# Optimization experiments

Measured on AMD Instinct MI355X. Metric: run time of the kernel, lower is better.

Reference implementation:

```python
import jax, jax.numpy as jnp
import numpy as np

# Sizes: B graphs, NPG nodes per graph (equal segments -> to_dense_batch == reshape),
# M instructions, DN node feat dim, DQ question dim.
B, NPG, M, DN, DQ = 64, 4096, 8, 512, 256
N = B * NPG
RATIO = 0.3
K = int(np.ceil(RATIO * NPG))  # pyg topk with ratio<1 keeps ceil(ratio*n) nodes per graph


def setup_inputs() -> dict:
    key = jax.random.key(0)
    ks = jax.random.split(key, 4)
    x = jax.random.normal(ks[0], (N, DN), jnp.float32)
    u = jax.random.normal(ks[1], (M, B, DQ), jnp.float32)
    Wn = jax.random.normal(ks[2], (DN, DQ), jnp.float32) / np.sqrt(DN)
    bn = jnp.zeros((DQ,), jnp.float32)
    batch = jnp.repeat(jnp.arange(B, dtype=jnp.int32), NPG)  # sorted graph ids, equal segments
    edge_index = jax.random.randint(ks[3], (2, 4 * N), 0, N, dtype=jnp.int32)  # unused by forward
    return {"x": x, "u": u, "Wn": Wn, "bn": bn, "batch": batch, "edge_index": edge_index}


def reference(x, u, Wn, bn, batch, edge_index):
    # node_nn: Linear(DN, DQ) + exact GELU (torch.nn.GELU default)
    h = jax.nn.gelu(x @ Wn + bn, approximate=False)            # [N, DQ]
    # to_dense_batch with equal-size graphs == reshape, mask all True
    hb = h.reshape(B, NPG, DQ)                                  # [B, n, D]
    inst = jnp.transpose(u, (1, 0, 2))                          # [B, M, D]
    scores = jnp.einsum('bmd,bnd->bmn', inst, hb)               # [B, M, n]
    attn = jax.nn.softmax(scores, axis=2)
    gate = attn.sum(axis=1)                                     # [B, n]  (gate[batch_mask] flatten)
    # per-graph ratio top-k -> hard binary mask (index_fill_ 1 at top-k, 0 elsewhere)
    kth = jax.lax.top_k(gate, K)[0][:, -1:]                     # k-th largest per graph
    mask = (gate >= kth).astype(h.dtype)                        # [B, n]
    return mask.reshape(N)
```

## Files before the change

### kernel.cpp

```cpp
#include <hip/hip_runtime.h>
#include <math.h>

#define B_     64
#define NPG_   4096
#define M_     8
#define DN_    512
#define DQ_    256
#define N_     (B_*NPG_)
#define KSEL_  1229

typedef _Float16 f16x4  __attribute__((ext_vector_type(4)));
typedef _Float16 f16x8  __attribute__((ext_vector_type(8)));
typedef float    f32x16 __attribute__((ext_vector_type(16)));

__global__ __launch_bounds__(256) void k_prep(const float* __restrict__ Wn,
                                              _Float16* __restrict__ th,
                                              _Float16* __restrict__ tl)
{
    const int k = blockIdx.x;
    const int c = threadIdx.x;
    const float w = Wn[k * DQ_ + c];
    const _Float16 h = (_Float16)w;
    th[c * DN_ + k] = h;
    tl[c * DN_ + k] = (_Float16)(w - (float)h);
}

__global__ __launch_bounds__(256, 2) void k_score(
    const float* __restrict__ x, const float* __restrict__ u,
    const float* __restrict__ bn,
    const _Float16* __restrict__ wth, const _Float16* __restrict__ wtl,
    float* __restrict__ scores)
{
    __shared__ __align__(16) _Float16 Ahi[128][40], Alo[128][40];
    __shared__ __align__(16) _Float16 Bhi[256][40], Blo[256][40];
    __shared__ float usS[M_][DQ_];
    __shared__ float bnsS[DQ_];
    __shared__ float part2[2][128][M_];

    const int tid = threadIdx.x;
    const int ln  = tid & 63;
    const int w   = tid >> 6;
    const int wr  = w >> 1;
    const int wc  = w & 1;
    const int lr  = ln & 31;
    const int lh  = ln >> 5;
    const int row0 = blockIdx.x * 128;
    const int b    = row0 >> 12;

    #pragma unroll
    for (int p = 0; p < 8; ++p) {
        const int idx = p * 256 + tid;
        usS[idx >> 8][idx & 255] = u[((idx >> 8) * B_ + b) * DQ_ + (idx & 255)];
    }
    bnsS[tid] = bn[tid];

    const int arow = tid >> 1;
    const int aks  = (tid & 1) * 16;
    const float*  xp  = x + (long)(row0 + arow) * DN_ + aks;
    const float4* bhp = (const float4*)(wth + (long)tid * DN_);
    const float4* blp = (const float4*)(wtl + (long)tid * DN_);

    float4 xa[4], bh[4], bl[4];
    #pragma unroll
    for (int i = 0; i < 4; ++i) {
        xa[i] = ((const float4*)xp)[i];
        bh[i] = bhp[i];
        bl[i] = blp[i];
    }

    f32x16 acc[2][4];
    #pragma unroll
    for (int mt = 0; mt < 2; ++mt)
        #pragma unroll
        for (int nt = 0; nt < 4; ++nt)
            #pragma unroll
            for (int r = 0; r < 16; ++r) acc[mt][nt][r] = 0.0f;

    for (int kt = 0; kt < DN_ / 32; ++kt) {
        __syncthreads();

        #pragma unroll
        for (int i = 0; i < 4; ++i) {
            const float4 v = xa[i];
            f16x4 h, lo2;
            h[0] = (_Float16)v.x; lo2[0] = (_Float16)(v.x - (float)h[0]);
            h[1] = (_Float16)v.y; lo2[1] = (_Float16)(v.y - (float)h[1]);
            h[2] = (_Float16)v.z; lo2[2] = (_Float16)(v.z - (float)h[2]);
            h[3] = (_Float16)v.w; lo2[3] = (_Float16)(v.w - (float)h[3]);
            *(f16x4*)&Ahi[arow][aks + 4 * i] = h;
            *(f16x4*)&Alo[arow][aks + 4 * i] = lo2;
        }
        #pragma unroll
        for (int i = 0; i < 4; ++i) {
            *(float4*)&Bhi[tid][i * 8] = bh[i];
            *(float4*)&Blo[tid][i * 8] = bl[i];
        }
        __syncthreads();

        if (kt + 1 < DN_ / 32) {
            const float* xn = xp + (kt + 1) * 32;
            #pragma unroll
            for (int i = 0; i < 4; ++i) {
                xa[i] = ((const float4*)xn)[i];
                bh[i] = bhp[(kt + 1) * 4 + i];
                bl[i] = blp[(kt + 1) * 4 + i];
            }
        }

        #pragma unroll
        for (int s = 0; s < 2; ++s) {
            const int o = s * 16 + lh * 8;
            f16x8 afh[2], afl[2], bfh[4], bfl[4];
            #pragma unroll
            for (int mt = 0; mt < 2; ++mt) {
                const int r = wr * 64 + mt * 32 + lr;
                afh[mt] = *(const f16x8*)&Ahi[r][o];
                afl[mt] = *(const f16x8*)&Alo[r][o];
            }
            #pragma unroll
            for (int nt = 0; nt < 4; ++nt) {
                const int c = wc * 128 + nt * 32 + lr;
                bfh[nt] = *(const f16x8*)&Bhi[c][o];
                bfl[nt] = *(const f16x8*)&Blo[c][o];
            }
            #pragma unroll
            for (int mt = 0; mt < 2; ++mt)
                #pragma unroll
                for (int nt = 0; nt < 4; ++nt) {
                    acc[mt][nt] = __builtin_amdgcn_mfma_f32_32x32x16_f16(
                        afh[mt], bfh[nt], acc[mt][nt], 0, 0, 0);
                    acc[mt][nt] = __builtin_amdgcn_mfma_f32_32x32x16_f16(
                        afh[mt], bfl[nt], acc[mt][nt], 0, 0, 0);
                    acc[mt][nt] = __builtin_amdgcn_mfma_f32_32x32x16_f16(
                        afl[mt], bfh[nt], acc[mt][nt], 0, 0, 0);
                }
        }
    }

    #pragma unroll
    for (int mt = 0; mt < 2; ++mt)
        #pragma unroll
        for (int nt = 0; nt < 4; ++nt) {
            const float bnc = bnsS[wc * 128 + nt * 32 + lr];
            #pragma unroll
            for (int r = 0; r < 16; ++r) {
                const float z = acc[mt][nt][r] + bnc;
                acc[mt][nt][r] = 0.5f * z * (1.0f + erff(z * 0.7071067811865476f));
            }
        }

    #pragma unroll 1
    for (int m = 0; m < 8; ++m) {
        const float u0 = usS[m][wc * 128 +   0 + lr];
        const float u1 = usS[m][wc * 128 +  32 + lr];
        const float u2 = usS[m][wc * 128 +  64 + lr];
        const float u3 = usS[m][wc * 128 +  96 + lr];
        float p[2][16];
        #pragma unroll
        for (int mt = 0; mt < 2; ++mt)
            #pragma unroll
            for (int r = 0; r < 16; ++r)
                p[mt][r] = acc[mt][0][r] * u0 + acc[mt][1][r] * u1
                         + acc[mt][2][r] * u2 + acc[mt][3][r] * u3;
        #pragma unroll
        for (int mask = 1; mask < 32; mask <<= 1)
            #pragma unroll
            for (int mt = 0; mt < 2; ++mt)
                #pragma unroll
                for (int r = 0; r < 16; ++r)
                    p[mt][r] += __shfl_xor(p[mt][r], mask, 64);
        if (lr == m) {
            #pragma unroll
            for (int mt = 0; mt < 2; ++mt)
                #pragma unroll
                for (int r = 0; r < 16; ++r) {
                    const int row = wr * 64 + mt * 32 + (r & 3) + 8 * (r >> 2) + 4 * lh;
                    part2[wc][row][m] = p[mt][r];
                }
        }
    }
    __syncthreads();

    #pragma unroll
    for (int i = 0; i < 4; ++i) {
        const int idx = i * 256 + tid;
        const int row = idx >> 3, m = idx & 7;
        scores[(long)(row0 + row) * M_ + m] = part2[0][row][m] + part2[1][row][m];
    }
}

__global__ __launch_bounds__(256) void k_mask(
    const float* __restrict__ scores, float* __restrict__ out)
{
    __shared__ float red[256];
    __shared__ float gateLDS[NPG_];
    __shared__ float gmaxS[M_];
    __shared__ float ginvS[M_];
    __shared__ unsigned hist[256];
    __shared__ unsigned sPrefix;
    __shared__ int sWant;

    const int b   = blockIdx.x;
    const int tid = threadIdx.x;
    const float* sb = scores + (long)b * NPG_ * M_;

    float lmax[8];
    #pragma unroll
    for (int m = 0; m < 8; ++m) lmax[m] = -INFINITY;
    for (int it = 0; it < 16; ++it) {
        const int n = it * 256 + tid;
        const float4 s0 = *(const float4*)(sb + (long)n * 8);
        const float4 s1 = *(const float4*)(sb + (long)n * 8 + 4);
        lmax[0] = fmaxf(lmax[0], s0.x); lmax[1] = fmaxf(lmax[1], s0.y);
        lmax[2] = fmaxf(lmax[2], s0.z); lmax[3] = fmaxf(lmax[3], s0.w);
        lmax[4] = fmaxf(lmax[4], s1.x); lmax[5] = fmaxf(lmax[5], s1.y);
        lmax[6] = fmaxf(lmax[6], s1.z); lmax[7] = fmaxf(lmax[7], s1.w);
    }
    for (int m = 0; m < 8; ++m) {
        red[tid] = lmax[m]; __syncthreads();
        for (int s = 128; s > 0; s >>= 1) {
            if (tid < s) red[tid] = fmaxf(red[tid], red[tid + s]);
            __syncthreads();
        }
        if (tid == 0) gmaxS[m] = red[0];
        __syncthreads();
    }

    float lsum[8];
    #pragma unroll
    for (int m = 0; m < 8; ++m) lsum[m] = 0.0f;
    for (int it = 0; it < 16; ++it) {
        const int n = it * 256 + tid;
        const float4 s0 = *(const float4*)(sb + (long)n * 8);
        const float4 s1 = *(const float4*)(sb + (long)n * 8 + 4);
        lsum[0] += expf(s0.x - gmaxS[0]); lsum[1] += expf(s0.y - gmaxS[1]);
        lsum[2] += expf(s0.z - gmaxS[2]); lsum[3] += expf(s0.w - gmaxS[3]);
        lsum[4] += expf(s1.x - gmaxS[4]); lsum[5] += expf(s1.y - gmaxS[5]);
        lsum[6] += expf(s1.z - gmaxS[6]); lsum[7] += expf(s1.w - gmaxS[7]);
    }
    for (int m = 0; m < 8; ++m) {
        red[tid] = lsum[m]; __syncthreads();
        for (int s = 128; s > 0; s >>= 1) {
            if (tid < s) red[tid] += red[tid + s];
            __syncthreads();
        }
        if (tid == 0) ginvS[m] = 1.0f / red[0];
        __syncthreads();
    }

    for (int it = 0; it < 16; ++it) {
        const int n = it * 256 + tid;
        const float4 s0 = *(const float4*)(sb + (long)n * 8);
        const float4 s1 = *(const float4*)(sb + (long)n * 8 + 4);
        float g = 0.0f;
        g += expf(s0.x - gmaxS[0]) * ginvS[0];
        g += expf(s0.y - gmaxS[1]) * ginvS[1];
        g += expf(s0.z - gmaxS[2]) * ginvS[2];
        g += expf(s0.w - gmaxS[3]) * ginvS[3];
        g += expf(s1.x - gmaxS[4]) * ginvS[4];
        g += expf(s1.y - gmaxS[5]) * ginvS[5];
        g += expf(s1.z - gmaxS[6]) * ginvS[6];
        g += expf(s1.w - gmaxS[7]) * ginvS[7];
        gateLDS[n] = g;
    }
    __syncthreads();

    if (tid == 0) { sPrefix = 0u; sWant = KSEL_; }
    __syncthreads();
    const unsigned himask[4] = {0u, 0xFF000000u, 0xFFFF0000u, 0xFFFFFF00u};
    for (int r = 0; r < 4; ++r) {
        hist[tid] = 0u;
        __syncthreads();
        const unsigned pfx = sPrefix;
        const unsigned hm  = himask[r];
        const int shift = 24 - 8 * r;
        for (int it = 0; it < 16; ++it) {
            const unsigned uv = __float_as_uint(gateLDS[it * 256 + tid]);
            if ((uv & hm) == pfx)
                atomicAdd(&hist[(uv >> shift) & 255u], 1u);
        }
        __syncthreads();
        if (tid == 0) {
            int want = sWant;
            unsigned acc = 0u;
            for (int bb = 255; bb >= 0; --bb) {
                const unsigned h = hist[bb];
                if (acc + h >= (unsigned)want) {
                    sWant   = want - (int)acc;
                    sPrefix = pfx | ((unsigned)bb << shift);
                    break;
                }
                acc += h;
            }
        }
        __syncthreads();
    }
    const float kth = __uint_as_float(sPrefix);

    for (int it = 0; it < 16; ++it) {
        const int n = it * 256 + tid;
        out[(long)b * NPG_ + n] = (gateLDS[n] >= kth) ? 1.0f : 0.0f;
    }
}

extern "C" void kernel_launch(void* const* d_in, const int* in_sizes, int n_in,
                              void* d_out, int out_size, void* d_ws, size_t ws_size,
                              hipStream_t stream) {
    const float* x  = (const float*)d_in[0];
    const float* u  = (const float*)d_in[1];
    const float* Wn = (const float*)d_in[2];
    const float* bn = (const float*)d_in[3];

    float* scores = (float*)d_ws;

    _Float16* wth = (_Float16*)d_out;
    _Float16* wtl = wth + DQ_ * DN_;
    float* out    = (float*)d_out;

    k_prep <<<DN_, 256, 0, stream>>>(Wn, wth, wtl);
    k_score<<<N_ / 128, 256, 0, stream>>>(x, u, bn, wth, wtl, scores);
    k_mask <<<B_, 256, 0, stream>>>(scores, out);
}
```

Before: 1.392 ms.

## Halve score-kernel row tile and widen mask kernel with wave-shuffle reductions

The score kernel now processes 64 rows per block, with each of four waves owning a 64-column slice of the output, which reduces accumulator registers and doubles the grid. Cross-wave partial scores are combined through reused B-tile shared memory. The mask kernel moves to 1024 threads and replaces the tree reductions in shared memory with wave shuffles plus a small cross-wave pass. The trade-off is higher B-tile reload traffic and more LDS reads and shuffles per MFMA in exchange for better occupancy.

Measured after the change: 1.394 ms. No clear change (+0.1%).

```diff
diff --git a/kernel.cpp b/kernel.cpp
--- a/kernel.cpp
+++ b/kernel.cpp
@@ -31,20 +31,18 @@
     const _Float16* __restrict__ wth, const _Float16* __restrict__ wtl,
     float* __restrict__ scores)
 {
-    __shared__ __align__(16) _Float16 Ahi[128][40], Alo[128][40];
+    __shared__ __align__(16) _Float16 Ahi[64][40],  Alo[64][40];
     __shared__ __align__(16) _Float16 Bhi[256][40], Blo[256][40];
     __shared__ float usS[M_][DQ_];
     __shared__ float bnsS[DQ_];
-    __shared__ float part2[2][128][M_];
+    float* part4f = (float*)&Bhi[0][0];
 
     const int tid = threadIdx.x;
     const int ln  = tid & 63;
-    const int w   = tid >> 6;
-    const int wr  = w >> 1;
-    const int wc  = w & 1;
+    const int wc  = tid >> 6;
     const int lr  = ln & 31;
     const int lh  = ln >> 5;
-    const int row0 = blockIdx.x * 128;
+    const int row0 = blockIdx.x * 64;
     const int b    = row0 >> 12;
 
     #pragma unroll
@@ -54,79 +52,79 @@
     }
     bnsS[tid] = bn[tid];
 
-    const int arow = tid >> 1;
-    const int aks  = (tid & 1) * 16;
-    const float*  xp  = x + (long)(row0 + arow) * DN_ + aks;
+    const int arow  = tid >> 2;
+    const int akoff = (tid & 3) * 8;
+    const float*  xp  = x + (long)(row0 + arow) * DN_ + akoff;
     const float4* bhp = (const float4*)(wth + (long)tid * DN_);
     const float4* blp = (const float4*)(wtl + (long)tid * DN_);
 
-    float4 xa[4], bh[4], bl[4];
-    #pragma unroll
-    for (int i = 0; i < 4; ++i) {
-        xa[i] = ((const float4*)xp)[i];
-        bh[i] = bhp[i];
-        bl[i] = blp[i];
-    }
-
-    f32x16 acc[2][4];
+    float4 xa[2], bh[4], bl[4];
+    #pragma unroll
+    for (int i = 0; i < 2; ++i) xa[i] = ((const float4*)xp)[i];
+    #pragma unroll
+    for (int j = 0; j < 4; ++j) { bh[j] = bhp[j]; bl[j] = blp[j]; }
+
+    f32x16 acc[2][2];
     #pragma unroll
     for (int mt = 0; mt < 2; ++mt)
         #pragma unroll
-        for (int nt = 0; nt < 4; ++nt)
+        for (int nt = 0; nt < 2; ++nt)
             #pragma unroll
             for (int r = 0; r < 16; ++r) acc[mt][nt][r] = 0.0f;
 
     for (int kt = 0; kt < DN_ / 32; ++kt) {
         __syncthreads();
 
-        #pragma unroll
-        for (int i = 0; i < 4; ++i) {
-            const float4 v = xa[i];
-            f16x4 h, lo2;
-            h[0] = (_Float16)v.x; lo2[0] = (_Float16)(v.x - (float)h[0]);
-            h[1] = (_Float16)v.y; lo2[1] = (_Float16)(v.y - (float)h[1]);
-            h[2] = (_Float16)v.z; lo2[2] = (_Float16)(v.z - (float)h[2]);
-            h[3] = (_Float16)v.w; lo2[3] = (_Float16)(v.w - (float)h[3]);
-            *(f16x4*)&Ahi[arow][aks + 4 * i] = h;
-            *(f16x4*)&Alo[arow][aks + 4 * i] = lo2;
-        }
-        #pragma unroll
-        for (int i = 0; i < 4; ++i) {
-            *(float4*)&Bhi[tid][i * 8] = bh[i];
-            *(float4*)&Blo[tid][i * 8] = bl[i];
+        {
+            f16x8 h, l;
+            h[0] = (_Float16)xa[0].x; l[0] = (_Float16)(xa[0].x - (float)h[0]);
+            h[1] = (_Float16)xa[0].y; l[1] = (_Float16)(xa[0].y - (float)h[1]);
+            h[2] = (_Float16)xa[0].z; l[2] = (_Float16)(xa[0].z - (float)h[2]);
+            h[3] = (_Float16)xa[0].w; l[3] = (_Float16)(xa[0].w - (float)h[3]);
+            h[4] = (_Float16)xa[1].x; l[4] = (_Float16)(xa[1].x - (float)h[4]);
+            h[5] = (_Float16)xa[1].y; l[5] = (_Float16)(xa[1].y - (float)h[5]);
+            h[6] = (_Float16)xa[1].z; l[6] = (_Float16)(xa[1].z - (float)h[6]);
+            h[7] = (_Float16)xa[1].w; l[7] = (_Float16)(xa[1].w - (float)h[7]);
+            *(f16x8*)&Ahi[arow][akoff] = h;
+            *(f16x8*)&Alo[arow][akoff] = l;
+        }
+        #pragma unroll
+        for (int j = 0; j < 4; ++j) {
+            *(float4*)&Bhi[tid][j * 8] = bh[j];
+            *(float4*)&Blo[tid][j * 8] = bl[j];
         }
         __syncthreads();
 
         if (kt + 1 < DN_ / 32) {
             const float* xn = xp + (kt + 1) * 32;
             #pragma unroll
-            for (int i = 0; i < 4; ++i) {
-                xa[i] = ((const float4*)xn)[i];
-                bh[i] = bhp[(kt + 1) * 4 + i];
-                bl[i] = blp[(kt + 1) * 4 + i];
+            for (int i = 0; i < 2; ++i) xa[i] = ((const float4*)xn)[i];
+            #pragma unroll
+            for (int j = 0; j < 4; ++j) {
+                bh[j] = bhp[(kt + 1) * 4 + j];
+                bl[j] = blp[(kt + 1) * 4 + j];
             }
         }
 
         #pragma unroll
         for (int s = 0; s < 2; ++s) {
             const int o = s * 16 + lh * 8;
-            f16x8 afh[2], afl[2], bfh[4], bfl[4];
+            f16x8 afh[2], afl[2], bfh[2], bfl[2];
             #pragma unroll
             for (int mt = 0; mt < 2; ++mt) {
-                const int r = wr * 64 + mt * 32 + lr;
-                afh[mt] = *(const f16x8*)&Ahi[r][o];
-                afl[mt] = *(const f16x8*)&Alo[r][o];
-            }
-            #pragma unroll
-            for (int nt = 0; nt < 4; ++nt) {
-                const int c = wc * 128 + nt * 32 + lr;
+                afh[mt] = *(const f16x8*)&Ahi[mt * 32 + lr][o];
+                afl[mt] = *(const f16x8*)&Alo[mt * 32 + lr][o];
+            }
+            #pragma unroll
+            for (int nt = 0; nt < 2; ++nt) {
+                const int c = wc * 64 + nt * 32 + lr;
                 bfh[nt] = *(const f16x8*)&Bhi[c][o];
                 bfl[nt] = *(const f16x8*)&Blo[c][o];
             }
             #pragma unroll
             for (int mt = 0; mt < 2; ++mt)
                 #pragma unroll
-                for (int nt = 0; nt < 4; ++nt) {
+                for (int nt = 0; nt < 2; ++nt) {
                     acc[mt][nt] = __builtin_amdgcn_mfma_f32_32x32x16_f16(
                         afh[mt], bfh[nt], acc[mt][nt], 0, 0, 0);
                     acc[mt][nt] = __builtin_amdgcn_mfma_f32_32x32x16_f16(
@@ -140,8 +138,8 @@
     #pragma unroll
     for (int mt = 0; mt < 2; ++mt)
         #pragma unroll
-        for (int nt = 0; nt < 4; ++nt) {
-            const float bnc = bnsS[wc * 128 + nt * 32 + lr];
+        for (int nt = 0; nt < 2; ++nt) {
+            const float bnc = bnsS[wc * 64 + nt * 32 + lr];
             #pragma unroll
             for (int r = 0; r < 16; ++r) {
                 const float z = acc[mt][nt][r] + bnc;
@@ -149,19 +147,18 @@
             }
         }
 
+    __syncthreads();
+
     #pragma unroll 1
     for (int m = 0; m < 8; ++m) {
-        const float u0 = usS[m][wc * 128 +   0 + lr];
-        const float u1 = usS[m][wc * 128 +  32 + lr];
-        const float u2 = usS[m][wc * 128 +  64 + lr];
-        const float u3 = usS[m][wc * 128 +  96 + lr];
+        const float u0 = usS[m][wc * 64 +  0 + lr];
+        const float u1 = usS[m][wc * 64 + 32 + lr];
         float p[2][16];
         #pragma unroll
         for (int mt = 0; mt < 2; ++mt)
             #pragma unroll
             for (int r = 0; r < 16; ++r)
-                p[mt][r] = acc[mt][0][r] * u0 + acc[mt][1][r] * u1
-                         + acc[mt][2][r] * u2 + acc[mt][3][r] * u3;
+                p[mt][r] = acc[mt][0][r] * u0 + acc[mt][1][r] * u1;
         #pragma unroll
         for (int mask = 1; mask < 32; mask <<= 1)
             #pragma unroll
@@ -174,108 +171,137 @@
             for (int mt = 0; mt < 2; ++mt)
                 #pragma unroll
                 for (int r = 0; r < 16; ++r) {
-                    const int row = wr * 64 + mt * 32 + (r & 3) + 8 * (r >> 2) + 4 * lh;
-                    part2[wc][row][m] = p[mt][r];
+                    const int row = mt * 32 + (r & 3) + 8 * (r >> 2) + 4 * lh;
+                    part4f[(wc * 64 + row) * M_ + m] = p[mt][r];
                 }
         }
     }
     __syncthreads();
 
     #pragma unroll
-    for (int i = 0; i < 4; ++i) {
+    for (int i = 0; i < 2; ++i) {
         const int idx = i * 256 + tid;
         const int row = idx >> 3, m = idx & 7;
-        scores[(long)(row0 + row) * M_ + m] = part2[0][row][m] + part2[1][row][m];
+        const float v = part4f[(  0 + row) * M_ + m] + part4f[( 64 + row) * M_ + m]
+                      + part4f[(128 + row) * M_ + m] + part4f[(192 + row) * M_ + m];
+        scores[(long)(row0 + row) * M_ + m] = v;
     }
 }
 
-__global__ __launch_bounds__(256) void k_mask(
+__global__ __launch_bounds__(1024) void k_mask(
     const float* __restrict__ scores, float* __restrict__ out)
 {
-    __shared__ float red[256];
     __shared__ float gateLDS[NPG_];
+    __shared__ float wred[16][M_];
     __shared__ float gmaxS[M_];
     __shared__ float ginvS[M_];
     __shared__ unsigned hist[256];
     __shared__ unsigned sPrefix;
     __shared__ int sWant;
 
-    const int b   = blockIdx.x;
-    const int tid = threadIdx.x;
+    const int b    = blockIdx.x;
+    const int tid  = threadIdx.x;
+    const int wid  = tid >> 6;
+    const int lane = tid & 63;
     const float* sb = scores + (long)b * NPG_ * M_;
 
-    float lmax[8];
-    #pragma unroll
-    for (int m = 0; m < 8; ++m) lmax[m] = -INFINITY;
-    for (int it = 0; it < 16; ++it) {
-        const int n = it * 256 + tid;
+    float lv[8];
+    #pragma unroll
+    for (int m = 0; m < 8; ++m) lv[m] = -INFINITY;
+    #pragma unroll
+    for (int it = 0; it < 4; ++it) {
+        const int n = it * 1024 + tid;
         const float4 s0 = *(const float4*)(sb + (long)n * 8);
         const float4 s1 = *(const float4*)(sb + (long)n * 8 + 4);
-        lmax[0] = fmaxf(lmax[0], s0.x); lmax[1] = fmaxf(lmax[1], s0.y);
-        lmax[2] = fmaxf(lmax[2], s0.z); lmax[3] = fmaxf(lmax[3], s0.w);
-        lmax[4] = fmaxf(lmax[4], s1.x); lmax[5] = fmaxf(lmax[5], s1.y);
-        lmax[6] = fmaxf(lmax[6], s1.z); lmax[7] = fmaxf(lmax[7], s1.w);
-    }
-    for (int m = 0; m < 8; ++m) {
-        red[tid] = lmax[m]; __syncthreads();
-        for (int s = 128; s > 0; s >>= 1) {
-            if (tid < s) red[tid] = fmaxf(red[tid], red[tid + s]);
-            __syncthreads();
-        }
-        if (tid == 0) gmaxS[m] = red[0];
-        __syncthreads();
-    }
-
-    float lsum[8];
-    #pragma unroll
-    for (int m = 0; m < 8; ++m) lsum[m] = 0.0f;
-    for (int it = 0; it < 16; ++it) {
-        const int n = it * 256 + tid;
+        lv[0] = fmaxf(lv[0], s0.x); lv[1] = fmaxf(lv[1], s0.y);
+        lv[2] = fmaxf(lv[2], s0.z); lv[3] = fmaxf(lv[3], s0.w);
+        lv[4] = fmaxf(lv[4], s1.x); lv[5] = fmaxf(lv[5], s1.y);
+        lv[6] = fmaxf(lv[6], s1.z); lv[7] = fmaxf(lv[7], s1.w);
+    }
+    #pragma unroll
+    for (int mask = 1; mask < 64; mask <<= 1)
+        #pragma unroll
+        for (int m = 0; m < 8; ++m)
+            lv[m] = fmaxf(lv[m], __shfl_xor(lv[m], mask, 64));
+    if (lane == 0)
+        #pragma unroll
+        for (int m = 0; m < 8; ++m) wred[wid][m] = lv[m];
+    __syncthreads();
+    if (tid < 8) {
+        float mm = -INFINITY;
+        for (int wv = 0; wv < 16; ++wv) mm = fmaxf(mm, wred[wv][tid]);
+        gmaxS[tid] = mm;
+    }
+    __syncthreads();
+
+    float gm[8];
+    #pragma unroll
+    for (int m = 0; m < 8; ++m) gm[m] = gmaxS[m];
+
+    float ls[8];
+    #pragma unroll
+    for (int m = 0; m < 8; ++m) ls[m] = 0.0f;
+    #pragma unroll
+    for (int it = 0; it < 4; ++it) {
+        const int n = it * 1024 + tid;
         const float4 s0 = *(const float4*)(sb + (long)n * 8);
         const float4 s1 = *(const float4*)(sb + (long)n * 8 + 4);
-        lsum[0] += expf(s0.x - gmaxS[0]); lsum[1] += expf(s0.y - gmaxS[1]);
-        lsum[2] += expf(s0.z - gmaxS[2]); lsum[3] += expf(s0.w - gmaxS[3]);
-        lsum[4] += expf(s1.x - gmaxS[4]); lsum[5] += expf(s1.y - gmaxS[5]);
-        lsum[6] += expf(s1.z - gmaxS[6]); lsum[7] += expf(s1.w - gmaxS[7]);
-    }
-    for (int m = 0; m < 8; ++m) {
-        red[tid] = lsum[m]; __syncthreads();
-        for (int s = 128; s > 0; s >>= 1) {
-            if (tid < s) red[tid] += red[tid + s];
-            __syncthreads();
-        }
-        if (tid == 0) ginvS[m] = 1.0f / red[0];
-        __syncthreads();
-    }
-
-    for (int it = 0; it < 16; ++it) {
-        const int n = it * 256 + tid;
+        ls[0] += expf(s0.x - gm[0]); ls[1] += expf(s0.y - gm[1]);
+        ls[2] += expf(s0.z - gm[2]); ls[3] += expf(s0.w - gm[3]);
+        ls[4] += expf(s1.x - gm[4]); ls[5] += expf(s1.y - gm[5]);
+        ls[6] += expf(s1.z - gm[6]); ls[7] += expf(s1.w - gm[7]);
+    }
+    #pragma unroll
+    for (int mask = 1; mask < 64; mask <<= 1)
+        #pragma unroll
+        for (int m = 0; m < 8; ++m)
+            ls[m] += __shfl_xor(ls[m], mask, 64);
+    if (lane == 0)
+        #pragma unroll
+        for (int m = 0; m < 8; ++m) wred[wid][m] = ls[m];
+    __syncthreads();
+    if (tid < 8) {
+        float ss = 0.0f;
+        for (int wv = 0; wv < 16; ++wv) ss += wred[wv][tid];
+        ginvS[tid] = 1.0f / ss;
+    }
+    __syncthreads();
+
+    float gi[8];
+    #pragma unroll
+    for (int m = 0; m < 8; ++m) gi[m] = ginvS[m];
+
+    #pragma unroll
+    for (int it = 0; it < 4; ++it) {
+        const int n = it * 1024 + tid;
         const float4 s0 = *(const float4*)(sb + (long)n * 8);
         const float4 s1 = *(const float4*)(sb + (long)n * 8 + 4);
         float g = 0.0f;
-        g += expf(s0.x - gmaxS[0]) * ginvS[0];
-        g += expf(s0.y - gmaxS[1]) * ginvS[1];
-        g += expf(s0.z - gmaxS[2]) * ginvS[2];
-        g += expf(s0.w - gmaxS[3]) * ginvS[3];
-        g += expf(s1.x - gmaxS[4]) * ginvS[4];
-        g += expf(s1.y - gmaxS[5]) * ginvS[5];
-        g += expf(s1.z - gmaxS[6]) * ginvS[6];
-        g += expf(s1.w - gmaxS[7]) * ginvS[7];
+        g += expf(s0.x - gm[0]) * gi[0];
+        g += expf(s0.y - gm[1]) * gi[1];
+        g += expf(s0.z - gm[2]) * gi[2];
+        g += expf(s0.w - gm[3]) * gi[3];
+        g += expf(s1.x - gm[4]) * gi[4];
+        g += expf(s1.y - gm[5]) * gi[5];
+        g += expf(s1.z - gm[6]) * gi[6];
+        g += expf(s1.w - gm[7]) * gi[7];
         gateLDS[n] = g;
     }
-    __syncthreads();
-
     if (tid == 0) { sPrefix = 0u; sWant = KSEL_; }
     __syncthreads();
-    const unsigned himask[4] = {0u, 0xFF000000u, 0xFFFF0000u, 0xFFFFFF00u};
+
+    #pragma unroll 1
     for (int r = 0; r < 4; ++r) {
-        hist[tid] = 0u;
+        if (tid < 256) hist[tid] = 0u;
         __syncthreads();
         const unsigned pfx = sPrefix;
-        const unsigned hm  = himask[r];
+        const unsigned hm  = (r == 0) ? 0u :
+                             (r == 1) ? 0xFF000000u :
+                             (r == 2) ? 0xFFFF0000u : 0xFFFFFF00u;
         const int shift = 24 - 8 * r;
-        for (int it = 0; it < 16; ++it) {
-            const unsigned uv = __float_as_uint(gateLDS[it * 256 + tid]);
+        #pragma unroll
+        for (int it = 0; it < 4; ++it) {
+            const unsigned uv = __float_as_uint(gateLDS[it * 1024 + tid]);
             if ((uv & hm) == pfx)
                 atomicAdd(&hist[(uv >> shift) & 255u], 1u);
         }
@@ -297,8 +323,9 @@
     }
     const float kth = __uint_as_float(sPrefix);
 
-    for (int it = 0; it < 16; ++it) {
-        const int n = it * 256 + tid;
+    #pragma unroll
+    for (int it = 0; it < 4; ++it) {
+        const int n = it * 1024 + tid;
         out[(long)b * NPG_ + n] = (gateLDS[n] >= kth) ? 1.0f : 0.0f;
     }
 }
@@ -318,6 +345,6 @@
     float* out    = (float*)d_out;
 
     k_prep <<<DN_, 256, 0, stream>>>(Wn, wth, wtl);
-    k_score<<<N_ / 128, 256, 0, stream>>>(x, u, bn, wth, wtl, scores);
-    k_mask <<<B_, 256, 0, stream>>>(scores, out);
+    k_score<<<N_ / 64, 256, 0, stream>>>(x, u, bn, wth, wtl, scores);
+    k_mask <<<B_, 1024, 0, stream>>>(scores, out);
 }
```
